# Kernel optimization log

Measured on AMD Instinct MI355X. Metric: run time of the kernel, lower is better.

The kernel has to match this reference:

```python
import jax, jax.numpy as jnp
import numpy as np

# AdaptiveLogSoftmaxWithLoss config (input_dim=2048, n_classes=50257, div_value=4.0)
CUTOFFS = [1000, 10000, 50257]  # torch appends n_classes
N_CLUSTERS = 2                   # len(CUTOFFS) - 1
HEAD_SIZE = CUTOFFS[0] + N_CLUSTERS  # 1002
D = 2048
HSZ = [D // 4, D // 16]          # tail hidden sizes: [512, 128]
N_TOK = 4096


def setup_inputs() -> dict:
    key = jax.random.key(0)
    ks = jax.random.split(key, 7)
    w = 0.02  # weight scale so logits stay O(1)
    x = jax.random.normal(ks[0], (N_TOK, D), dtype=jnp.float32)
    W_head = jax.random.normal(ks[1], (HEAD_SIZE, D), dtype=jnp.float32) * w
    W1_0 = jax.random.normal(ks[2], (HSZ[0], D), dtype=jnp.float32) * w
    W2_0 = jax.random.normal(ks[3], (CUTOFFS[1] - CUTOFFS[0], HSZ[0]), dtype=jnp.float32) * w  # [9000, 512]
    W1_1 = jax.random.normal(ks[4], (HSZ[1], D), dtype=jnp.float32) * w
    W2_1 = jax.random.normal(ks[5], (CUTOFFS[2] - CUTOFFS[1], HSZ[1]), dtype=jnp.float32) * w  # [40257, 128]
    target = jax.random.randint(ks[6], (N_TOK,), 0, CUTOFFS[2], dtype=jnp.int32)
    return {"x": x, "target": target, "W_head": W_head,
            "W1_0": W1_0, "W2_0": W2_0, "W1_1": W1_1, "W2_1": W2_1}


def reference(x, target, W_head, W1_0, W2_0, W1_1, W2_1):
    # head: [N, 1002] = [1000 frequent classes | 2 cluster logits]
    head = x @ W_head.T
    head_lsm = jax.nn.log_softmax(head, axis=-1)

    t = target
    # log-prob of target if it lies in the head (clip keeps gather in-range; masked later)
    head_lp = jnp.take_along_axis(head_lsm, jnp.clip(t, 0, CUTOFFS[0] - 1)[:, None], axis=1)[:, 0]

    def tail_target_lp(W1, W2, low, high, cluster_idx):
        # two-stage projection: [N,D] @ [D,h] @ [h,osz]
        logits = (x @ W1.T) @ W2.T                     # [N, high-low]
        lsm = jax.nn.log_softmax(logits, axis=-1)
        idx = jnp.clip(t - low, 0, high - low - 1)
        g = jnp.take_along_axis(lsm, idx[:, None], axis=1)[:, 0]
        # combine with head's cluster log-prob
        return head_lsm[:, CUTOFFS[0] + cluster_idx] + g

    lp0 = tail_target_lp(W1_0, W2_0, CUTOFFS[0], CUTOFFS[1], 0)
    lp1 = tail_target_lp(W1_1, W2_1, CUTOFFS[1], CUTOFFS[2], 1)

    out = jnp.where(t < CUTOFFS[0], head_lp, jnp.where(t < CUTOFFS[1], lp0, lp1))
    loss = -jnp.mean(out)
    return out, loss
```

## Files before the change

kernel.cpp:

```cpp
#include <hip/hip_runtime.h>
#include <hip/hip_bf16.h>
#include <math.h>

#define NTOK 4096
#define DIM 2048
#define NHEAD 1002
#define NCAT 1664
#define C0LO 1000
#define C0HI 10000
#define OSZ0 9000
#define OSZ1 40257
#define H0S 512
#define H1S 128
#define JS0 16
#define JS1 16
#define HEADBLKS 8

typedef __attribute__((ext_vector_type(4))) short short4v;
typedef __attribute__((ext_vector_type(8))) short short8v;
typedef __attribute__((ext_vector_type(4))) float f32x4;
typedef __hip_bfloat16 bf16;

#define GLOBAL_AS __attribute__((address_space(1)))
#define LDS_AS __attribute__((address_space(3)))

#define RAW_BAR() __builtin_amdgcn_s_barrier()
#define SCHED_FENCE() __builtin_amdgcn_sched_barrier(0)
#define WAIT_VM(N) asm volatile("s_waitcnt vmcnt(" #N ")" ::: "memory")
#define WAIT_LGKM0() asm volatile("s_waitcnt lgkmcnt(0)" ::: "memory")

__global__ __launch_bounds__(256) void cvt_all(
    const float* __restrict__ x, const float* __restrict__ W_head,
    const float* __restrict__ W1_0, const float* __restrict__ W1_1,
    const float* __restrict__ W2_0, const float* __restrict__ W2_1,
    bf16* __restrict__ xb, bf16* __restrict__ Wcat,
    bf16* __restrict__ W20b, bf16* __restrict__ W21b) {
  const long NX = (long)NTOK * DIM / 8;
  const long NC = (long)NCAT * DIM / 8;
  const long N20 = (long)OSZ0 * H0S / 8;
  const long N21 = (long)OSZ1 * H1S / 8;
  long gid = (long)blockIdx.x * 256 + threadIdx.x;
  const float* src = nullptr;
  bf16* dst;
  if (gid < NX) {
    src = x + gid * 8; dst = xb + gid * 8;
  } else if (gid < NX + NC) {
    long o = (gid - NX) * 8;
    int row = (int)(o >> 11), k = (int)(o & 2047);
    dst = Wcat + o;
    if (row < NHEAD) src = W_head + (long)row * DIM + k;
    else if (row < 1024) src = nullptr;
    else if (row < 1536) src = W1_0 + (long)(row - 1024) * DIM + k;
    else src = W1_1 + (long)(row - 1536) * DIM + k;
  } else if (gid < NX + NC + N20) {
    long o = (gid - NX - NC) * 8; src = W2_0 + o; dst = W20b + o;
  } else if (gid < NX + NC + N20 + N21) {
    long o = (gid - NX - NC - N20) * 8; src = W2_1 + o; dst = W21b + o;
  } else {
    return;
  }
  union { short8v v; bf16 h[8]; } u;
  if (src) {
    float4 a = *reinterpret_cast<const float4*>(src);
    float4 b = *reinterpret_cast<const float4*>(src + 4);
    u.h[0] = __float2bfloat16(a.x); u.h[1] = __float2bfloat16(a.y);
    u.h[2] = __float2bfloat16(a.z); u.h[3] = __float2bfloat16(a.w);
    u.h[4] = __float2bfloat16(b.x); u.h[5] = __float2bfloat16(b.y);
    u.h[6] = __float2bfloat16(b.z); u.h[7] = __float2bfloat16(b.w);
  } else {
#pragma unroll
    for (int e = 0; e < 8; ++e) u.h[e] = __float2bfloat16(0.f);
  }
  *reinterpret_cast<short8v*>(dst) = u.v;
}

__device__ __forceinline__ void stage_tile(const bf16* __restrict__ g, int row0,
                                           int maxrow, int ld, int k0,
                                           char* lds, int wave, int lane) {
#pragma unroll
  for (int c = 0; c < 4; ++c) {
    int rbase = wave * 32 + c * 8;
    int row = rbase + (lane >> 3);
    int grow = row0 + row;
    grow = grow < maxrow ? grow : maxrow;
    int slot = (lane & 7) ^ (row & 7);
    const bf16* src = g + (size_t)grow * ld + k0 + slot * 8;
    __builtin_amdgcn_global_load_lds((const GLOBAL_AS unsigned int*)src,
                                     (LDS_AS unsigned int*)(lds + rbase * 128),
                                     16, 0, 0);
  }
}

__device__ __forceinline__ short8v read_frag(const char* lds, int row, int kk, int lane) {
  int g = lane >> 4;
  int r7 = row & 7;
  int b1 = kk * 64 + g * 8;
  int b2 = b1 + 32;
  b1 = ((b1 >> 4) ^ r7) * 16 + (b1 & 15);
  b2 = ((b2 >> 4) ^ r7) * 16 + (b2 & 15);
  const char* p = lds + row * 128;
  short4v lo = *reinterpret_cast<const short4v*>(p + b1);
  short4v hi = *reinterpret_cast<const short4v*>(p + b2);
  return __builtin_shufflevector(lo, hi, 0, 1, 2, 3, 4, 5, 6, 7);
}

__device__ __forceinline__ void stage_tile256(const bf16* __restrict__ g, int row0,
                                              int maxrow, int ld,
                                              char* lds, int wave, int lane) {
#pragma unroll
  for (int c = 0; c < 8; ++c) {
    int rbase = wave * 32 + c * 4;
    int row = rbase + (lane >> 4);
    int grow = row0 + row;
    grow = grow < maxrow ? grow : maxrow;
    int slot = (lane & 15) ^ (row & 7);
    const bf16* src = g + (size_t)grow * ld + slot * 8;
    __builtin_amdgcn_global_load_lds((const GLOBAL_AS unsigned int*)src,
                                     (LDS_AS unsigned int*)(lds + rbase * 256),
                                     16, 0, 0);
  }
}

__device__ __forceinline__ short8v read_frag256(const char* lds, int row, int kk, int lane) {
  int g = lane >> 4;
  int r7 = row & 7;
  int b1 = kk * 64 + g * 8;
  int b2 = b1 + 32;
  b1 = (((b1 >> 4) ^ r7) << 4) | (b1 & 15);
  b2 = (((b2 >> 4) ^ r7) << 4) | (b2 & 15);
  const char* p = lds + row * 256;
  short4v lo = *reinterpret_cast<const short4v*>(p + b1);
  short4v hi = *reinterpret_cast<const short4v*>(p + b2);
  return __builtin_shufflevector(lo, hi, 0, 1, 2, 3, 4, 5, 6, 7);
}

__global__ __launch_bounds__(256, 2) void proj_gemm(
    const bf16* __restrict__ A, const bf16* __restrict__ B,
    float* __restrict__ head, float* __restrict__ h0, bf16* __restrict__ h0b,
    float* __restrict__ h1, bf16* __restrict__ h1b, float* __restrict__ ps_head) {
  __shared__ __align__(16) char As[128 * 128];
  __shared__ __align__(16) char Bs[128 * 128];
  __shared__ float reds[128];
  int tid = threadIdx.x;
  int lane = tid & 63, wave = tid >> 6;
  int wr = wave >> 1, wc = wave & 1;
  int row0 = blockIdx.y * 128, col0 = blockIdx.x * 128;
  f32x4 acc[4][4] = {};
  for (int k0 = 0; k0 < DIM; k0 += 64) {
    __syncthreads();
    stage_tile(A, row0, NTOK - 1, DIM, k0, As, wave, lane);
    stage_tile(B, col0, NCAT - 1, DIM, k0, Bs, wave, lane);
    __syncthreads();
#pragma unroll
    for (int kk = 0; kk < 2; ++kk) {
      short8v af[4], bfr[4];
#pragma unroll
      for (int m = 0; m < 4; ++m)
        af[m] = read_frag(As, wr * 64 + m * 16 + (lane & 15), kk, lane);
#pragma unroll
      for (int n = 0; n < 4; ++n)
        bfr[n] = read_frag(Bs, wc * 64 + n * 16 + (lane & 15), kk, lane);
#pragma unroll
      for (int m = 0; m < 4; ++m)
#pragma unroll
        for (int n = 0; n < 4; ++n)
          acc[m][n] = __builtin_amdgcn_mfma_f32_16x16x32_bf16(af[m], bfr[n], acc[m][n], 0, 0, 0);
    }
  }
  float srun[4][4] = {};
#pragma unroll
  for (int m = 0; m < 4; ++m) {
    int row = row0 + wr * 64 + m * 16 + (lane >> 4) * 4;
#pragma unroll
    for (int n = 0; n < 4; ++n) {
      int col = col0 + wc * 64 + n * 16 + (lane & 15);
#pragma unroll
      for (int r = 0; r < 4; ++r) {
        float v = acc[m][n][r];
        if (col < NHEAD) {
          head[(size_t)(row + r) * NHEAD + col] = v;
          srun[m][r] += __expf(v);
        } else if (col >= 1024 && col < 1536) {
          h0[(size_t)(row + r) * H0S + (col - 1024)] = v;
          h0b[(size_t)(row + r) * H0S + (col - 1024)] = __float2bfloat16(v);
        } else if (col >= 1536) {
          h1[(size_t)(row + r) * H1S + (col - 1536)] = v;
          h1b[(size_t)(row + r) * H1S + (col - 1536)] = __float2bfloat16(v);
        }
      }
    }
  }
  if (blockIdx.x < HEADBLKS) {
#pragma unroll
    for (int off = 1; off < 16; off <<= 1)
#pragma unroll
      for (int m = 0; m < 4; ++m)
#pragma unroll
        for (int r = 0; r < 4; ++r) srun[m][r] += __shfl_xor(srun[m][r], off);
    __syncthreads();
    if (wc == 0 && (lane & 15) == 0) {
#pragma unroll
      for (int m = 0; m < 4; ++m)
#pragma unroll
        for (int r = 0; r < 4; ++r)
          reds[wr * 64 + m * 16 + (lane >> 4) * 4 + r] = srun[m][r];
    }
    __syncthreads();
    if (wc == 1 && (lane & 15) == 0) {
#pragma unroll
      for (int m = 0; m < 4; ++m)
#pragma unroll
        for (int r = 0; r < 4; ++r) {
          int row = wr * 64 + m * 16 + (lane >> 4) * 4 + r;
          ps_head[(size_t)blockIdx.x * NTOK + row0 + row] = reds[row] + srun[m][r];
        }
    }
  }
}

template <int H, int OSZ, int JSPLIT>
__global__ __launch_bounds__(256, 2) void tail_lse_mfma(
    const bf16* __restrict__ Ab, const bf16* __restrict__ W2b,
    float* __restrict__ ps) {
  __shared__ __align__(16) char As[128 * 128];
  __shared__ __align__(16) char Bs[128 * 128];
  __shared__ float reds[128];
  int tid = threadIdx.x;
  int lane = tid & 63, wave = tid >> 6;
  int wr = wave >> 1, wc = wave & 1;
  int tok0 = blockIdx.x * 128;
  const int NT = (OSZ + 127) / 128;
  const int TPS = (NT + JSPLIT - 1) / JSPLIT;
  int t_lo = blockIdx.y * TPS;
  int t_hi = min(NT, t_lo + TPS);
  float srun[4][4] = {};
  for (int jt = t_lo; jt < t_hi; ++jt) {
    int j0 = jt * 128;
    f32x4 acc[4][4] = {};
    for (int k0 = 0; k0 < H; k0 += 64) {
      __syncthreads();
      stage_tile(Ab, tok0, NTOK - 1, H, k0, As, wave, lane);
      stage_tile(W2b, j0, OSZ - 1, H, k0, Bs, wave, lane);
      __syncthreads();
#pragma unroll
      for (int kk = 0; kk < 2; ++kk) {
        short8v af[4], bfr[4];
#pragma unroll
        for (int m = 0; m < 4; ++m)
          af[m] = read_frag(As, wr * 64 + m * 16 + (lane & 15), kk, lane);
#pragma unroll
        for (int n = 0; n < 4; ++n)
          bfr[n] = read_frag(Bs, wc * 64 + n * 16 + (lane & 15), kk, lane);
#pragma unroll
        for (int m = 0; m < 4; ++m)
#pragma unroll
          for (int n = 0; n < 4; ++n)
            acc[m][n] = __builtin_amdgcn_mfma_f32_16x16x32_bf16(af[m], bfr[n], acc[m][n], 0, 0, 0);
      }
    }
#pragma unroll
    for (int m = 0; m < 4; ++m)
#pragma unroll
      for (int n = 0; n < 4; ++n) {
        int col = j0 + wc * 64 + n * 16 + (lane & 15);
        if (col < OSZ) {
#pragma unroll
          for (int r = 0; r < 4; ++r) srun[m][r] += __expf(acc[m][n][r]);
        }
      }
  }
#pragma unroll
  for (int off = 1; off < 16; off <<= 1)
#pragma unroll
    for (int m = 0; m < 4; ++m)
#pragma unroll
      for (int r = 0; r < 4; ++r) srun[m][r] += __shfl_xor(srun[m][r], off);
  __syncthreads();
  if (wc == 0 && (lane & 15) == 0) {
#pragma unroll
    for (int m = 0; m < 4; ++m)
#pragma unroll
      for (int r = 0; r < 4; ++r)
        reds[wr * 64 + m * 16 + (lane >> 4) * 4 + r] = srun[m][r];
  }
  __syncthreads();
  if (wc == 1 && (lane & 15) == 0) {
#pragma unroll
    for (int m = 0; m < 4; ++m)
#pragma unroll
      for (int r = 0; r < 4; ++r) {
        int row = wr * 64 + m * 16 + (lane >> 4) * 4 + r;
        ps[(size_t)blockIdx.y * NTOK + tok0 + row] = reds[row] + srun[m][r];
      }
  }
}

__global__ __launch_bounds__(256, 2) void tail1_lse(
    const bf16* __restrict__ Ab, const bf16* __restrict__ W2b,
    float* __restrict__ ps) {
  __shared__ __align__(16) char ldsA[32 * 1024];
  __shared__ __align__(16) char ldsB[32 * 1024];
  __shared__ float reds[128];
  int tid = threadIdx.x;
  int lane = tid & 63, wave = tid >> 6;
  int wr = wave >> 1, wc = wave & 1;
  int tok0 = blockIdx.x * 128;
  const int NT = (OSZ1 + 127) / 128;
  const int TPS = (NT + JS1 - 1) / JS1;
  int t_lo = blockIdx.y * TPS;
  int t_hi = min(NT, t_lo + TPS);
  int nt = t_hi - t_lo;

  stage_tile256(Ab, tok0, NTOK - 1, H1S, ldsA, wave, lane);
  WAIT_VM(0); SCHED_FENCE();
  RAW_BAR();
  short8v afr[4][4];
#pragma unroll
  for (int kk = 0; kk < 4; ++kk)
#pragma unroll
    for (int m = 0; m < 4; ++m)
      afr[kk][m] = read_frag256(ldsA, wr * 64 + m * 16 + (lane & 15), kk, lane);
  stage_tile256(W2b, t_lo * 128, OSZ1 - 1, H1S, ldsB, wave, lane);
  WAIT_LGKM0(); SCHED_FENCE();
  RAW_BAR();
  if (nt > 1) stage_tile256(W2b, (t_lo + 1) * 128, OSZ1 - 1, H1S, ldsA, wave, lane);

  float srun[4][4] = {};
  for (int i = 0; i < nt; ++i) {
    char* cur = (i & 1) ? ldsA : ldsB;
    if (i + 1 < nt) { WAIT_VM(8); } else { WAIT_VM(0); }
    SCHED_FENCE();
    RAW_BAR();
    int j0 = (t_lo + i) * 128;
    f32x4 acc[4][4] = {};
#pragma unroll
    for (int kk = 0; kk < 4; ++kk) {
      short8v bfr[4];
#pragma unroll
      for (int n = 0; n < 4; ++n)
        bfr[n] = read_frag256(cur, wc * 64 + n * 16 + (lane & 15), kk, lane);
#pragma unroll
      for (int m = 0; m < 4; ++m)
#pragma unroll
        for (int n = 0; n < 4; ++n)
          acc[m][n] = __builtin_amdgcn_mfma_f32_16x16x32_bf16(afr[kk][m], bfr[n], acc[m][n], 0, 0, 0);
    }
#pragma unroll
    for (int m = 0; m < 4; ++m)
#pragma unroll
      for (int n = 0; n < 4; ++n) {
        int col = j0 + wc * 64 + n * 16 + (lane & 15);
        if (col < OSZ1) {
#pragma unroll
          for (int r = 0; r < 4; ++r) srun[m][r] += __expf(acc[m][n][r]);
        }
      }
    SCHED_FENCE();
    RAW_BAR();
    if (i + 2 < nt) stage_tile256(W2b, (t_lo + i + 2) * 128, OSZ1 - 1, H1S, cur, wave, lane);
  }
#pragma unroll
  for (int off = 1; off < 16; off <<= 1)
#pragma unroll
    for (int m = 0; m < 4; ++m)
#pragma unroll
      for (int r = 0; r < 4; ++r) srun[m][r] += __shfl_xor(srun[m][r], off);
  __syncthreads();
  if (wc == 0 && (lane & 15) == 0) {
#pragma unroll
    for (int m = 0; m < 4; ++m)
#pragma unroll
      for (int r = 0; r < 4; ++r)
        reds[wr * 64 + m * 16 + (lane >> 4) * 4 + r] = srun[m][r];
  }
  __syncthreads();
  if (wc == 1 && (lane & 15) == 0) {
#pragma unroll
    for (int m = 0; m < 4; ++m)
#pragma unroll
      for (int r = 0; r < 4; ++r) {
        int row = wr * 64 + m * 16 + (lane >> 4) * 4 + r;
        ps[(size_t)blockIdx.y * NTOK + tok0 + row] = reds[row] + srun[m][r];
      }
  }
}

__global__ __launch_bounds__(256) void finalize2(
    const int* __restrict__ target, const float* __restrict__ head,
    const float* __restrict__ ps_head,
    const float* __restrict__ h0, const float* __restrict__ h1,
    const float* __restrict__ W2_0, const float* __restrict__ W2_1,
    const float* __restrict__ ps0, const float* __restrict__ ps1,
    float* __restrict__ out) {
  int warp = threadIdx.x >> 6, lane = threadIdx.x & 63;
  int i = blockIdx.x * 4 + warp;
  if (i >= NTOK) return;
  int t = target[i];
  float sh = 0.f;
#pragma unroll
  for (int s = 0; s < HEADBLKS; ++s) sh += ps_head[(size_t)s * NTOK + i];
  float lse_head = logf(sh);
  float res;
  if (t < C0LO) {
    res = head[(size_t)i * NHEAD + t] - lse_head;
  } else {
    int c = (t < C0HI) ? 0 : 1;
    int H = c ? H1S : H0S;
    int low = c ? C0HI : C0LO;
    const float* hv = (c ? h1 : h0) + (size_t)i * H;
    const float* wv = (c ? W2_1 : W2_0) + (size_t)(t - low) * H;
    float p = 0.f;
    for (int k = lane * 4; k < H; k += 256) {
      float4 a = *reinterpret_cast<const float4*>(hv + k);
      float4 b = *reinterpret_cast<const float4*>(wv + k);
      p += a.x * b.x + a.y * b.y + a.z * b.z + a.w * b.w;
    }
#pragma unroll
    for (int off = 32; off > 0; off >>= 1) p += __shfl_xor(p, off);
    const float* ps = c ? ps1 : ps0;
    float S = 0.f;
    for (int s = 0; s < JS0; ++s) S += ps[(size_t)s * NTOK + i];
    float cl = head[(size_t)i * NHEAD + C0LO + c];
    res = (cl - lse_head) + (p - logf(S));
  }
  if (lane == 0) out[i] = res;
}

__global__ __launch_bounds__(256) void loss_kernel(float* __restrict__ out) {
  __shared__ float red[256];
  int tid = threadIdx.x;
  float s = 0.f;
  for (int j = tid; j < NTOK; j += 256) s += out[j];
  red[tid] = s; __syncthreads();
  for (int off = 128; off > 0; off >>= 1) {
    if (tid < off) red[tid] += red[tid + off];
    __syncthreads();
  }
  if (tid == 0) out[NTOK] = -red[0] / (float)NTOK;
}

extern "C" void kernel_launch(void* const* d_in, const int* in_sizes, int n_in,
                              void* d_out, int out_size, void* d_ws, size_t ws_size,
                              hipStream_t stream) {
  (void)in_sizes; (void)n_in; (void)out_size; (void)ws_size;
  const float* x = (const float*)d_in[0];
  const int* target = (const int*)d_in[1];
  const float* W_head = (const float*)d_in[2];
  const float* W1_0 = (const float*)d_in[3];
  const float* W2_0 = (const float*)d_in[4];
  const float* W1_1 = (const float*)d_in[5];
  const float* W2_1 = (const float*)d_in[6];
  float* out = (float*)d_out;

  char* w = (char*)d_ws;
  size_t off = 0;
  auto alloc = [&](size_t bytes) -> void* {
    void* p = w + off;
    off = (off + bytes + 255) & ~(size_t)255;
    return p;
  };
  bf16* xb   = (bf16*)alloc((size_t)NTOK * DIM * 2);
  bf16* Wcat = (bf16*)alloc((size_t)NCAT * DIM * 2);
  bf16* W20b = (bf16*)alloc((size_t)OSZ0 * H0S * 2);
  bf16* W21b = (bf16*)alloc((size_t)OSZ1 * H1S * 2);
  float* head = (float*)alloc((size_t)NTOK * NHEAD * 4);
  float* h0   = (float*)alloc((size_t)NTOK * H0S * 4);
  bf16*  h0b  = (bf16*)alloc((size_t)NTOK * H0S * 2);
  float* h1   = (float*)alloc((size_t)NTOK * H1S * 4);
  bf16*  h1b  = (bf16*)alloc((size_t)NTOK * H1S * 2);
  float* ps_head = (float*)alloc((size_t)HEADBLKS * NTOK * 4);
  float* ps0 = (float*)alloc((size_t)JS0 * NTOK * 4);
  float* ps1 = (float*)alloc((size_t)JS1 * NTOK * 4);

  dim3 blk(256);
  const long TOT8 = (long)NTOK * DIM / 8 + (long)NCAT * DIM / 8 +
                    (long)OSZ0 * H0S / 8 + (long)OSZ1 * H1S / 8;
  cvt_all<<<dim3((unsigned)((TOT8 + 255) / 256)), blk, 0, stream>>>(
      x, W_head, W1_0, W1_1, W2_0, W2_1, xb, Wcat, W20b, W21b);

  proj_gemm<<<dim3(NCAT / 128, NTOK / 128), blk, 0, stream>>>(
      xb, Wcat, head, h0, h0b, h1, h1b, ps_head);

  tail_lse_mfma<H0S, OSZ0, JS0><<<dim3(NTOK / 128, JS0), blk, 0, stream>>>(h0b, W20b, ps0);
  tail1_lse<<<dim3(NTOK / 128, JS1), blk, 0, stream>>>(h1b, W21b, ps1);

  finalize2<<<dim3(NTOK / 4), blk, 0, stream>>>(target, head, ps_head, h0, h1,
                                                W2_0, W2_1, ps0, ps1, out);
  loss_kernel<<<1, blk, 0, stream>>>(out);
}
```

Before: 195.1 us.

## Double-buffer proj and tail0 GEMMs and fuse both tail kernels into one launch

The projection GEMM and the tail-0 log-sum-exp GEMM now use double-buffered LDS with asynchronous staging two steps ahead and vmcnt waits, replacing the stage/sync/compute loop. The two tail kernels are merged into one launch that dispatches on block index, so both clusters run concurrently and one launch is saved. Tile splits switch to balanced floor division. LDS per block grows to about 64KB, which can reduce occupancy.

```diff
diff --git a/kernel.cpp b/kernel.cpp
--- a/kernel.cpp
+++ b/kernel.cpp
@@ -15,6 +15,9 @@
 #define JS0 16
 #define JS1 16
 #define HEADBLKS 8
+#define NB0 512
+#define NT0 71
+#define NT1 315
 
 typedef __attribute__((ext_vector_type(4))) short short4v;
 typedef __attribute__((ext_vector_type(8))) short short8v;
@@ -134,37 +137,226 @@
   return __builtin_shufflevector(lo, hi, 0, 1, 2, 3, 4, 5, 6, 7);
 }
 
-__global__ __launch_bounds__(256, 2) void proj_gemm(
+__device__ __forceinline__ void reduce_write_ps(float srun[4][4], float* reds,
+                                                float* ps, int slice, int tok0,
+                                                int lane, int wr, int wc) {
+#pragma unroll
+  for (int off = 1; off < 16; off <<= 1)
+#pragma unroll
+    for (int m = 0; m < 4; ++m)
+#pragma unroll
+      for (int r = 0; r < 4; ++r) srun[m][r] += __shfl_xor(srun[m][r], off);
+  __syncthreads();
+  if (wc == 0 && (lane & 15) == 0) {
+#pragma unroll
+    for (int m = 0; m < 4; ++m)
+#pragma unroll
+      for (int r = 0; r < 4; ++r)
+        reds[wr * 64 + m * 16 + (lane >> 4) * 4 + r] = srun[m][r];
+  }
+  __syncthreads();
+  if (wc == 1 && (lane & 15) == 0) {
+#pragma unroll
+    for (int m = 0; m < 4; ++m)
+#pragma unroll
+      for (int r = 0; r < 4; ++r) {
+        int row = wr * 64 + m * 16 + (lane >> 4) * 4 + r;
+        ps[(size_t)slice * NTOK + tok0 + row] = reds[row] + srun[m][r];
+      }
+  }
+}
+
+__device__ void tail0_path(const bf16* __restrict__ Ab, const bf16* __restrict__ W2b,
+                           float* __restrict__ ps, int bid, char* lds) {
+  char* Abuf[2] = {lds, lds + 16384};
+  char* Bbuf[2] = {lds + 32768, lds + 49152};
+  float* reds = (float*)(lds + 65536);
+  int tid = threadIdx.x;
+  int lane = tid & 63, wave = tid >> 6;
+  int wr = wave >> 1, wc = wave & 1;
+  int tb = bid & 31, ys = bid >> 5;
+  int tok0 = tb * 128;
+  int t_lo = (NT0 * ys) / JS0, t_hi = (NT0 * (ys + 1)) / JS0;
+  int niter = (t_hi - t_lo) * 8;
+
+  stage_tile(Ab, tok0, NTOK - 1, H0S, (0 & 7) * 64, Abuf[0], wave, lane);
+  stage_tile(W2b, (t_lo + 0) * 128, OSZ0 - 1, H0S, 0 * 64, Bbuf[0], wave, lane);
+  if (niter > 1) {
+    stage_tile(Ab, tok0, NTOK - 1, H0S, 1 * 64, Abuf[1], wave, lane);
+    stage_tile(W2b, t_lo * 128, OSZ0 - 1, H0S, 1 * 64, Bbuf[1], wave, lane);
+  }
+  float srun[4][4] = {};
+  f32x4 acc[4][4];
+  for (int it = 0; it < niter; ++it) {
+    char* Ac = Abuf[it & 1];
+    char* Bc = Bbuf[it & 1];
+    if (it + 1 < niter) { WAIT_VM(8); } else { WAIT_VM(0); }
+    SCHED_FENCE();
+    RAW_BAR();
+    int kst = it & 7;
+    if (kst == 0) {
+#pragma unroll
+      for (int m = 0; m < 4; ++m)
+#pragma unroll
+        for (int n = 0; n < 4; ++n) acc[m][n] = f32x4{0.f, 0.f, 0.f, 0.f};
+    }
+#pragma unroll
+    for (int kk = 0; kk < 2; ++kk) {
+      short8v af[4], bfr[4];
+#pragma unroll
+      for (int m = 0; m < 4; ++m)
+        af[m] = read_frag(Ac, wr * 64 + m * 16 + (lane & 15), kk, lane);
+#pragma unroll
+      for (int n = 0; n < 4; ++n)
+        bfr[n] = read_frag(Bc, wc * 64 + n * 16 + (lane & 15), kk, lane);
+#pragma unroll
+      for (int m = 0; m < 4; ++m)
+#pragma unroll
+        for (int n = 0; n < 4; ++n)
+          acc[m][n] = __builtin_amdgcn_mfma_f32_16x16x32_bf16(af[m], bfr[n], acc[m][n], 0, 0, 0);
+    }
+    if (kst == 7) {
+      int j0 = (t_lo + (it >> 3)) * 128;
+#pragma unroll
+      for (int m = 0; m < 4; ++m)
+#pragma unroll
+        for (int n = 0; n < 4; ++n) {
+          int col = j0 + wc * 64 + n * 16 + (lane & 15);
+          if (col < OSZ0) {
+#pragma unroll
+            for (int r = 0; r < 4; ++r) srun[m][r] += __expf(acc[m][n][r]);
+          }
+        }
+    }
+    SCHED_FENCE();
+    RAW_BAR();
+    if (it + 2 < niter) {
+      int it2 = it + 2;
+      stage_tile(Ab, tok0, NTOK - 1, H0S, (it2 & 7) * 64, Ac, wave, lane);
+      stage_tile(W2b, (t_lo + (it2 >> 3)) * 128, OSZ0 - 1, H0S, (it2 & 7) * 64, Bc, wave, lane);
+    }
+  }
+  reduce_write_ps(srun, reds, ps, ys, tok0, lane, wr, wc);
+}
+
+__device__ void tail1_path(const bf16* __restrict__ Ab, const bf16* __restrict__ W2b,
+                           float* __restrict__ ps, int bid, char* lds) {
+  char* buf0 = lds;
+  char* buf1 = lds + 32768;
+  float* reds = (float*)(lds + 65536);
+  int tid = threadIdx.x;
+  int lane = tid & 63, wave = tid >> 6;
+  int wr = wave >> 1, wc = wave & 1;
+  int tb = bid & 31, ys = bid >> 5;
+  int tok0 = tb * 128;
+  int t_lo = (NT1 * ys) / JS1, t_hi = (NT1 * (ys + 1)) / JS1;
+  int nt = t_hi - t_lo;
+
+  stage_tile256(Ab, tok0, NTOK - 1, H1S, buf1, wave, lane);
+  WAIT_VM(0); SCHED_FENCE();
+  RAW_BAR();
+  short8v afr[4][4];
+#pragma unroll
+  for (int kk = 0; kk < 4; ++kk)
+#pragma unroll
+    for (int m = 0; m < 4; ++m)
+      afr[kk][m] = read_frag256(buf1, wr * 64 + m * 16 + (lane & 15), kk, lane);
+  stage_tile256(W2b, t_lo * 128, OSZ1 - 1, H1S, buf0, wave, lane);
+  WAIT_LGKM0(); SCHED_FENCE();
+  RAW_BAR();
+  if (nt > 1) stage_tile256(W2b, (t_lo + 1) * 128, OSZ1 - 1, H1S, buf1, wave, lane);
+
+  float srun[4][4] = {};
+  for (int i = 0; i < nt; ++i) {
+    char* cur = (i & 1) ? buf1 : buf0;
+    if (i + 1 < nt) { WAIT_VM(8); } else { WAIT_VM(0); }
+    SCHED_FENCE();
+    RAW_BAR();
+    int j0 = (t_lo + i) * 128;
+    f32x4 acc[4][4] = {};
+#pragma unroll
+    for (int kk = 0; kk < 4; ++kk) {
+      short8v bfr[4];
+#pragma unroll
+      for (int n = 0; n < 4; ++n)
+        bfr[n] = read_frag256(cur, wc * 64 + n * 16 + (lane & 15), kk, lane);
+#pragma unroll
+      for (int m = 0; m < 4; ++m)
+#pragma unroll
+        for (int n = 0; n < 4; ++n)
+          acc[m][n] = __builtin_amdgcn_mfma_f32_16x16x32_bf16(afr[kk][m], bfr[n], acc[m][n], 0, 0, 0);
+    }
+#pragma unroll
+    for (int m = 0; m < 4; ++m)
+#pragma unroll
+      for (int n = 0; n < 4; ++n) {
+        int col = j0 + wc * 64 + n * 16 + (lane & 15);
+        if (col < OSZ1) {
+#pragma unroll
+          for (int r = 0; r < 4; ++r) srun[m][r] += __expf(acc[m][n][r]);
+        }
+      }
+    SCHED_FENCE();
+    RAW_BAR();
+    if (i + 2 < nt) stage_tile256(W2b, (t_lo + i + 2) * 128, OSZ1 - 1, H1S, cur, wave, lane);
+  }
+  reduce_write_ps(srun, reds, ps, ys, tok0, lane, wr, wc);
+}
+
+__global__ __launch_bounds__(256, 2) void tails_fused(
+    const bf16* __restrict__ h0b, const bf16* __restrict__ W20b,
+    const bf16* __restrict__ h1b, const bf16* __restrict__ W21b,
+    float* __restrict__ ps0, float* __restrict__ ps1) {
+  __shared__ __align__(16) char lds[66048];
+  int bid = blockIdx.x;
+  if (bid < NB0) tail0_path(h0b, W20b, ps0, bid, lds);
+  else           tail1_path(h1b, W21b, ps1, bid - NB0, lds);
+}
+
+__device__ void proj_gemm_body(
     const bf16* __restrict__ A, const bf16* __restrict__ B,
     float* __restrict__ head, float* __restrict__ h0, bf16* __restrict__ h0b,
-    float* __restrict__ h1, bf16* __restrict__ h1b, float* __restrict__ ps_head) {
-  __shared__ __align__(16) char As[128 * 128];
-  __shared__ __align__(16) char Bs[128 * 128];
-  __shared__ float reds[128];
+    float* __restrict__ h1, bf16* __restrict__ h1b, float* __restrict__ ps_head,
+    char* lds) {
+  char* Abuf[2] = {lds, lds + 16384};
+  char* Bbuf[2] = {lds + 32768, lds + 49152};
+  float* reds = (float*)(lds + 65536);
   int tid = threadIdx.x;
   int lane = tid & 63, wave = tid >> 6;
   int wr = wave >> 1, wc = wave & 1;
   int row0 = blockIdx.y * 128, col0 = blockIdx.x * 128;
+  const int NIT = DIM / 64;
+  stage_tile(A, row0, NTOK - 1, DIM, 0, Abuf[0], wave, lane);
+  stage_tile(B, col0, NCAT - 1, DIM, 0, Bbuf[0], wave, lane);
+  stage_tile(A, row0, NTOK - 1, DIM, 64, Abuf[1], wave, lane);
+  stage_tile(B, col0, NCAT - 1, DIM, 64, Bbuf[1], wave, lane);
   f32x4 acc[4][4] = {};
-  for (int k0 = 0; k0 < DIM; k0 += 64) {
-    __syncthreads();
-    stage_tile(A, row0, NTOK - 1, DIM, k0, As, wave, lane);
-    stage_tile(B, col0, NCAT - 1, DIM, k0, Bs, wave, lane);
-    __syncthreads();
+  for (int it = 0; it < NIT; ++it) {
+    char* Ac = Abuf[it & 1];
+    char* Bc = Bbuf[it & 1];
+    if (it + 1 < NIT) { WAIT_VM(8); } else { WAIT_VM(0); }
+    SCHED_FENCE();
+    RAW_BAR();
 #pragma unroll
     for (int kk = 0; kk < 2; ++kk) {
       short8v af[4], bfr[4];
 #pragma unroll
       for (int m = 0; m < 4; ++m)
-        af[m] = read_frag(As, wr * 64 + m * 16 + (lane & 15), kk, lane);
+        af[m] = read_frag(Ac, wr * 64 + m * 16 + (lane & 15), kk, lane);
 #pragma unroll
       for (int n = 0; n < 4; ++n)
-        bfr[n] = read_frag(Bs, wc * 64 + n * 16 + (lane & 15), kk, lane);
+        bfr[n] = read_frag(Bc, wc * 64 + n * 16 + (lane & 15), kk, lane);
 #pragma unroll
       for (int m = 0; m < 4; ++m)
 #pragma unroll
         for (int n = 0; n < 4; ++n)
           acc[m][n] = __builtin_amdgcn_mfma_f32_16x16x32_bf16(af[m], bfr[n], acc[m][n], 0, 0, 0);
+    }
+    SCHED_FENCE();
+    RAW_BAR();
+    if (it + 2 < NIT) {
+      stage_tile(A, row0, NTOK - 1, DIM, (it + 2) * 64, Ac, wave, lane);
+      stage_tile(B, col0, NCAT - 1, DIM, (it + 2) * 64, Bc, wave, lane);
     }
   }
   float srun[4][4] = {};
@@ -191,198 +383,16 @@
     }
   }
   if (blockIdx.x < HEADBLKS) {
-#pragma unroll
-    for (int off = 1; off < 16; off <<= 1)
-#pragma unroll
-      for (int m = 0; m < 4; ++m)
-#pragma unroll
-        for (int r = 0; r < 4; ++r) srun[m][r] += __shfl_xor(srun[m][r], off);
-    __syncthreads();
-    if (wc == 0 && (lane & 15) == 0) {
-#pragma unroll
-      for (int m = 0; m < 4; ++m)
-#pragma unroll
-        for (int r = 0; r < 4; ++r)
-          reds[wr * 64 + m * 16 + (lane >> 4) * 4 + r] = srun[m][r];
-    }
-    __syncthreads();
-    if (wc == 1 && (lane & 15) == 0) {
-#pragma unroll
-      for (int m = 0; m < 4; ++m)
-#pragma unroll
-        for (int r = 0; r < 4; ++r) {
-          int row = wr * 64 + m * 16 + (lane >> 4) * 4 + r;
-          ps_head[(size_t)blockIdx.x * NTOK + row0 + row] = reds[row] + srun[m][r];
-        }
-    }
-  }
-}
-
-template <int H, int OSZ, int JSPLIT>
-__global__ __launch_bounds__(256, 2) void tail_lse_mfma(
-    const bf16* __restrict__ Ab, const bf16* __restrict__ W2b,
-    float* __restrict__ ps) {
-  __shared__ __align__(16) char As[128 * 128];
-  __shared__ __align__(16) char Bs[128 * 128];
-  __shared__ float reds[128];
-  int tid = threadIdx.x;
-  int lane = tid & 63, wave = tid >> 6;
-  int wr = wave >> 1, wc = wave & 1;
-  int tok0 = blockIdx.x * 128;
-  const int NT = (OSZ + 127) / 128;
-  const int TPS = (NT + JSPLIT - 1) / JSPLIT;
-  int t_lo = blockIdx.y * TPS;
-  int t_hi = min(NT, t_lo + TPS);
-  float srun[4][4] = {};
-  for (int jt = t_lo; jt < t_hi; ++jt) {
-    int j0 = jt * 128;
-    f32x4 acc[4][4] = {};
-    for (int k0 = 0; k0 < H; k0 += 64) {
-      __syncthreads();
-      stage_tile(Ab, tok0, NTOK - 1, H, k0, As, wave, lane);
-      stage_tile(W2b, j0, OSZ - 1, H, k0, Bs, wave, lane);
-      __syncthreads();
-#pragma unroll
-      for (int kk = 0; kk < 2; ++kk) {
-        short8v af[4], bfr[4];
-#pragma unroll
-        for (int m = 0; m < 4; ++m)
-          af[m] = read_frag(As, wr * 64 + m * 16 + (lane & 15), kk, lane);
-#pragma unroll
-        for (int n = 0; n < 4; ++n)
-          bfr[n] = read_frag(Bs, wc * 64 + n * 16 + (lane & 15), kk, lane);
-#pragma unroll
-        for (int m = 0; m < 4; ++m)
-#pragma unroll
-          for (int n = 0; n < 4; ++n)
-            acc[m][n] = __builtin_amdgcn_mfma_f32_16x16x32_bf16(af[m], bfr[n], acc[m][n], 0, 0, 0);
-      }
-    }
-#pragma unroll
-    for (int m = 0; m < 4; ++m)
-#pragma unroll
-      for (int n = 0; n < 4; ++n) {
-        int col = j0 + wc * 64 + n * 16 + (lane & 15);
-        if (col < OSZ) {
-#pragma unroll
-          for (int r = 0; r < 4; ++r) srun[m][r] += __expf(acc[m][n][r]);
-        }
-      }
-  }
-#pragma unroll
-  for (int off = 1; off < 16; off <<= 1)
-#pragma unroll
-    for (int m = 0; m < 4; ++m)
-#pragma unroll
-      for (int r = 0; r < 4; ++r) srun[m][r] += __shfl_xor(srun[m][r], off);
-  __syncthreads();
-  if (wc == 0 && (lane & 15) == 0) {
-#pragma unroll
-    for (int m = 0; m < 4; ++m)
-#pragma unroll
-      for (int r = 0; r < 4; ++r)
-        reds[wr * 64 + m * 16 + (lane >> 4) * 4 + r] = srun[m][r];
-  }
-  __syncthreads();
-  if (wc == 1 && (lane & 15) == 0) {
-#pragma unroll
-    for (int m = 0; m < 4; ++m)
-#pragma unroll
-      for (int r = 0; r < 4; ++r) {
-        int row = wr * 64 + m * 16 + (lane >> 4) * 4 + r;
-        ps[(size_t)blockIdx.y * NTOK + tok0 + row] = reds[row] + srun[m][r];
-      }
-  }
-}
-
-__global__ __launch_bounds__(256, 2) void tail1_lse(
-    const bf16* __restrict__ Ab, const bf16* __restrict__ W2b,
-    float* __restrict__ ps) {
-  __shared__ __align__(16) char ldsA[32 * 1024];
-  __shared__ __align__(16) char ldsB[32 * 1024];
-  __shared__ float reds[128];
-  int tid = threadIdx.x;
-  int lane = tid & 63, wave = tid >> 6;
-  int wr = wave >> 1, wc = wave & 1;
-  int tok0 = blockIdx.x * 128;
-  const int NT = (OSZ1 + 127) / 128;
-  const int TPS = (NT + JS1 - 1) / JS1;
-  int t_lo = blockIdx.y * TPS;
-  int t_hi = min(NT, t_lo + TPS);
-  int nt = t_hi - t_lo;
-
-  stage_tile256(Ab, tok0, NTOK - 1, H1S, ldsA, wave, lane);
-  WAIT_VM(0); SCHED_FENCE();
-  RAW_BAR();
-  short8v afr[4][4];
-#pragma unroll
-  for (int kk = 0; kk < 4; ++kk)
-#pragma unroll
-    for (int m = 0; m < 4; ++m)
-      afr[kk][m] = read_frag256(ldsA, wr * 64 + m * 16 + (lane & 15), kk, lane);
-  stage_tile256(W2b, t_lo * 128, OSZ1 - 1, H1S, ldsB, wave, lane);
-  WAIT_LGKM0(); SCHED_FENCE();
-  RAW_BAR();
-  if (nt > 1) stage_tile256(W2b, (t_lo + 1) * 128, OSZ1 - 1, H1S, ldsA, wave, lane);
-
-  float srun[4][4] = {};
-  for (int i = 0; i < nt; ++i) {
-    char* cur = (i & 1) ? ldsA : ldsB;
-    if (i + 1 < nt) { WAIT_VM(8); } else { WAIT_VM(0); }
-    SCHED_FENCE();
-    RAW_BAR();
-    int j0 = (t_lo + i) * 128;
-    f32x4 acc[4][4] = {};
-#pragma unroll
-    for (int kk = 0; kk < 4; ++kk) {
-      short8v bfr[4];
-#pragma unroll
-      for (int n = 0; n < 4; ++n)
-        bfr[n] = read_frag256(cur, wc * 64 + n * 16 + (lane & 15), kk, lane);
-#pragma unroll
-      for (int m = 0; m < 4; ++m)
-#pragma unroll
-        for (int n = 0; n < 4; ++n)
-          acc[m][n] = __builtin_amdgcn_mfma_f32_16x16x32_bf16(afr[kk][m], bfr[n], acc[m][n], 0, 0, 0);
-    }
-#pragma unroll
-    for (int m = 0; m < 4; ++m)
-#pragma unroll
-      for (int n = 0; n < 4; ++n) {
-        int col = j0 + wc * 64 + n * 16 + (lane & 15);
-        if (col < OSZ1) {
-#pragma unroll
-          for (int r = 0; r < 4; ++r) srun[m][r] += __expf(acc[m][n][r]);
-        }
-      }
-    SCHED_FENCE();
-    RAW_BAR();
-    if (i + 2 < nt) stage_tile256(W2b, (t_lo + i + 2) * 128, OSZ1 - 1, H1S, cur, wave, lane);
-  }
-#pragma unroll
-  for (int off = 1; off < 16; off <<= 1)
-#pragma unroll
-    for (int m = 0; m < 4; ++m)
-#pragma unroll
-      for (int r = 0; r < 4; ++r) srun[m][r] += __shfl_xor(srun[m][r], off);
-  __syncthreads();
-  if (wc == 0 && (lane & 15) == 0) {
-#pragma unroll
-    for (int m = 0; m < 4; ++m)
-#pragma unroll
-      for (int r = 0; r < 4; ++r)
-        reds[wr * 64 + m * 16 + (lane >> 4) * 4 + r] = srun[m][r];
-  }
-  __syncthreads();
-  if (wc == 1 && (lane & 15) == 0) {
-#pragma unroll
-    for (int m = 0; m < 4; ++m)
-#pragma unroll
-      for (int r = 0; r < 4; ++r) {
-        int row = wr * 64 + m * 16 + (lane >> 4) * 4 + r;
-        ps[(size_t)blockIdx.y * NTOK + tok0 + row] = reds[row] + srun[m][r];
-      }
-  }
+    reduce_write_ps(srun, reds, ps_head, blockIdx.x, row0, lane, wr, wc);
+  }
+}
+
+__global__ __launch_bounds__(256, 2) void proj_gemm(
+    const bf16* __restrict__ A, const bf16* __restrict__ B,
+    float* __restrict__ head, float* __restrict__ h0, bf16* __restrict__ h0b,
+    float* __restrict__ h1, bf16* __restrict__ h1b, float* __restrict__ ps_head) {
+  __shared__ __align__(16) char lds[66048];
+  proj_gemm_body(A, B, head, h0, h0b, h1, h1b, ps_head, lds);
 }
 
 __global__ __launch_bounds__(256) void finalize2(
@@ -481,8 +491,7 @@
   proj_gemm<<<dim3(NCAT / 128, NTOK / 128), blk, 0, stream>>>(
       xb, Wcat, head, h0, h0b, h1, h1b, ps_head);
 
-  tail_lse_mfma<H0S, OSZ0, JS0><<<dim3(NTOK / 128, JS0), blk, 0, stream>>>(h0b, W20b, ps0);
-  tail1_lse<<<dim3(NTOK / 128, JS1), blk, 0, stream>>>(h1b, W21b, ps1);
+  tails_fused<<<dim3(NB0 + 32 * JS1), blk, 0, stream>>>(h0b, W20b, h1b, W21b, ps0, ps1);
 
   finalize2<<<dim3(NTOK / 4), blk, 0, stream>>>(target, head, ps_head, h0, h1,
                                                 W2_0, W2_1, ps0, ps1, out);
```

Result: slower. 247.1 us (+26.7%).
